# Kernel optimization log

Hardware: AMD Instinct MI355X
Metric: run time of the kernel (lower is better)

## Reference

```python
import jax, jax.numpy as jnp
import numpy as np

T, D, FF, E, R = 4096, 1024, 2048, 4, 16
LORA_SCALE = 32.0 / 16.0  # alpha / r


def setup_inputs() -> dict:
    key = jax.random.key(0)
    ks = jax.random.split(key, 12)
    return {
        "x": jax.random.normal(ks[0], (T, D), jnp.float32),
        "gate_w": jax.random.normal(ks[1], (E, D), jnp.float32) * 0.03,
        "gate_up_w": jax.random.normal(ks[2], (D, 2 * FF), jnp.float32)[None].repeat(E, 0) * 0.0
                     + jax.random.normal(ks[2], (E, D, 2 * FF), jnp.float32) * 0.03,
        "gate_up_b": jax.random.normal(ks[3], (E, 2 * FF), jnp.float32) * 0.01,
        "down_w": jax.random.normal(ks[4], (E, FF, D), jnp.float32) * 0.02,
        "down_b": jax.random.normal(ks[5], (E, D), jnp.float32) * 0.01,
        "A_gate": jax.random.normal(ks[6], (E, R, D), jnp.float32) * 0.02,
        "B_gate": jax.random.normal(ks[7], (E, FF, R), jnp.float32) * 0.02,
        "A_up": jax.random.normal(ks[8], (E, R, D), jnp.float32) * 0.02,
        "B_up": jax.random.normal(ks[9], (E, FF, R), jnp.float32) * 0.02,
        "A_down": jax.random.normal(ks[10], (E, R, FF), jnp.float32) * 0.02,
        "B_down": jax.random.normal(ks[11], (E, D, R), jnp.float32) * 0.02,
        "top_k": 2,
    }


def reference(x, gate_w, gate_up_w, gate_up_b, down_w, down_b,
              A_gate, B_gate, A_up, B_up, A_down, B_down, top_k):
    t, d = x.shape
    e = gate_w.shape[0]
    # --- router: logits, softmax (fp32), top-k, renormalize ---
    router_logits = x @ gate_w.T                                   # [T,E]
    rw = jax.nn.softmax(router_logits.astype(jnp.float32), axis=1)
    top_w, sel = jax.lax.top_k(rw, top_k)                          # [T,k]
    top_w = top_w / jnp.sum(top_w, axis=-1, keepdims=True)
    top_w = top_w.astype(x.dtype)
    # dense per-token per-expert combine weights (scatter of top-k weights)
    w = jnp.zeros((t, e), x.dtype).at[jnp.arange(t)[:, None], sel].add(top_w)  # [T,E]
    # --- per-expert SwiGLU MLP with LoRA (vectorized over experts) ---
    gu = jnp.einsum('td,edf->etf', x, gate_up_w) + gate_up_b[:, None, :]       # [E,T,2FF]
    ff = gu.shape[-1] // 2
    gate = gu[..., :ff] + jnp.einsum('td,erd,efr->etf', x, A_gate, B_gate) * LORA_SCALE
    up = gu[..., ff:] + jnp.einsum('td,erd,efr->etf', x, A_up, B_up) * LORA_SCALE
    act = jax.nn.silu(gate) * up                                               # [E,T,FF]
    down = jnp.einsum('etf,efd->etd', act, down_w) + down_b[:, None, :]
    down = down + jnp.einsum('etf,erf,edr->etd', act, A_down, B_down) * LORA_SCALE
    # --- weighted scatter-combine ---
    final = jnp.einsum('etd,te->td', down, w)                                  # [T,D]
    return final, router_logits
```

## Files before the change

kernel.cpp:

```cpp
#include <hip/hip_runtime.h>

#define T_TOK 4096
#define DIM   1024
#define FFD   2048
#define NEXP  4
#define NRP   8704
#define MTILES 68

typedef unsigned short u16;
typedef __attribute__((ext_vector_type(8))) short short8;
typedef __attribute__((ext_vector_type(4))) float f32x4;
typedef __attribute__((ext_vector_type(8))) unsigned short u16x8;
typedef __attribute__((ext_vector_type(4))) unsigned short u16x4;

typedef __attribute__((address_space(1))) unsigned int as1_u32;
typedef __attribute__((address_space(3))) unsigned int as3_u32;

__device__ __forceinline__ u16 f2bf(float f) {
  union { float f; unsigned u; } v; v.f = f;
  unsigned u = v.u;
  return (u16)((u + 0x7fffu + ((u >> 16) & 1u)) >> 16);
}
__device__ __forceinline__ float bf2f(u16 h) {
  union { unsigned u; float f; } v; v.u = ((unsigned)h) << 16;
  return v.f;
}
__device__ __forceinline__ void gload16(const void* g, void* l) {
  __builtin_amdgcn_global_load_lds((const as1_u32*)g, (as3_u32*)l, 16, 0, 0);
}

__global__ void router_k(const float* __restrict__ x, const float* __restrict__ gw,
                         float* __restrict__ logits_out, int* __restrict__ sel,
                         float* __restrict__ selw) {
  int t = blockIdx.x;
  int lane = threadIdx.x;
  float xv[16];
#pragma unroll
  for (int i = 0; i < 16; ++i) xv[i] = x[(size_t)t * DIM + lane + i * 64];
  float l[4];
#pragma unroll
  for (int e = 0; e < 4; ++e) {
    float s = 0.f;
#pragma unroll
    for (int i = 0; i < 16; ++i) s += xv[i] * gw[e * DIM + lane + i * 64];
#pragma unroll
    for (int off = 32; off > 0; off >>= 1) s += __shfl_xor(s, off, 64);
    l[e] = s;
  }
  if (lane == 0) {
#pragma unroll
    for (int e = 0; e < 4; ++e) logits_out[(size_t)t * 4 + e] = l[e];
    int e0 = 0; float b0 = l[0];
    for (int e = 1; e < 4; ++e) if (l[e] > b0) { b0 = l[e]; e0 = e; }
    int e1 = -1; float b1 = -3.4e38f;
    for (int e = 0; e < 4; ++e) if (e != e0 && l[e] > b1) { b1 = l[e]; e1 = e; }
    float p1 = expf(b1 - b0);
    float w0 = 1.f / (1.f + p1);
    sel[2 * t] = e0; sel[2 * t + 1] = e1;
    selw[2 * t] = w0; selw[2 * t + 1] = 1.f - w0;
  }
}

__global__ void scan_k(const int* __restrict__ sel, int* __restrict__ pos,
                       int* __restrict__ offs, int* __restrict__ rowtok,
                       int* __restrict__ pairrow) {
  __shared__ int base[4];
  __shared__ int wsum[16];
  __shared__ int off_s[5];
  int tid = threadIdx.x, lane = tid & 63, wid = tid >> 6;
  if (tid < 4) base[tid] = 0;
  __syncthreads();
  for (int chunk = 0; chunk < 4; ++chunk) {
    int t = chunk * 1024 + tid;
    int e0 = sel[2 * t], e1 = sel[2 * t + 1];
    for (int e = 0; e < 4; ++e) {
      bool f = (e0 == e) || (e1 == e);
      unsigned long long m = __ballot(f);
      int within = __popcll(m & ((1ull << lane) - 1ull));
      if (lane == 0) wsum[wid] = __popcll(m);
      __syncthreads();
      int wbase = 0, tot = 0;
      for (int i = 0; i < 16; ++i) { int v = wsum[i]; if (i < wid) wbase += v; tot += v; }
      if (f) {
        int p = base[e] + wbase + within;
        if (e0 == e) pos[2 * t] = p; else pos[2 * t + 1] = p;
      }
      __syncthreads();
      if (tid == 0) base[e] += tot;
      __syncthreads();
    }
  }
  if (tid == 0) {
    int o = 0;
    for (int e = 0; e < 4; ++e) { off_s[e] = o; o += ((base[e] + 127) >> 7) << 7; }
    off_s[4] = o;
    for (int i = 0; i < 5; ++i) offs[i] = off_s[i];
  }
  __syncthreads();
  for (int r = tid; r < NRP; r += 1024) rowtok[r] = -1;
  __syncthreads();
  for (int t = tid; t < T_TOK; t += 1024) {
#pragma unroll
    for (int s = 0; s < 2; ++s) {
      int e = sel[2 * t + s];
      int rr = off_s[e] + pos[2 * t + s];
      pairrow[2 * t + s] = rr;
      rowtok[rr] = t;
    }
  }
}

__global__ void gather_k(const float* __restrict__ x, const int* __restrict__ rowtok,
                         u16* __restrict__ xg) {
  int r = blockIdx.x, tid = threadIdx.x;
  int t = rowtok[r];
  float4 v = make_float4(0.f, 0.f, 0.f, 0.f);
  if (t >= 0) v = ((const float4*)(x + (size_t)t * DIM))[tid];
  u16x4 o;
  o[0] = f2bf(v.x); o[1] = f2bf(v.y); o[2] = f2bf(v.z); o[3] = f2bf(v.w);
  ((u16x4*)(xg + (size_t)r * DIM))[tid] = o;
}

__global__ void cvtA_k(const float* __restrict__ Ag, const float* __restrict__ Au,
                       const float* __restrict__ Ad, u16* __restrict__ abgu,
                       u16* __restrict__ adb) {
  int g = blockIdx.x * 256 + threadIdx.x;
  if (g < 32768) {
    int flat = g * 4;
    int e = flat >> 15;
    int rem = flat & 32767;
    int q = rem >> 10;
    int d = rem & 1023;
    const float* src = (q < 16) ? (Ag + ((size_t)e * 16 + q) * DIM + d)
                                : (Au + ((size_t)e * 16 + (q - 16)) * DIM + d);
    float4 v = *(const float4*)src;
    u16x4 o; o[0] = f2bf(v.x); o[1] = f2bf(v.y); o[2] = f2bf(v.z); o[3] = f2bf(v.w);
    *(u16x4*)(abgu + (size_t)flat) = o;
  } else {
    int flat = (g - 32768) * 4;
    float4 v = *(const float4*)(Ad + flat);
    u16x4 o; o[0] = f2bf(v.x); o[1] = f2bf(v.y); o[2] = f2bf(v.z); o[3] = f2bf(v.w);
    *(u16x4*)(adb + (size_t)flat) = o;
  }
}

__global__ void xa_k(const u16* __restrict__ xg, const u16* __restrict__ abgu,
                     const int* __restrict__ offs, float* __restrict__ xagu) {
  int r0 = blockIdx.x * 2, lane = threadIdx.x;
  int e = 0;
  if (r0 >= offs[1]) e = 1;
  if (r0 >= offs[2]) e = 2;
  if (r0 >= offs[3]) e = 3;
  float x0[16], x1[16];
#pragma unroll
  for (int i = 0; i < 4; ++i) {
    u16x4 v0 = ((const u16x4*)(xg + (size_t)r0 * DIM))[lane + i * 64];
    u16x4 v1 = ((const u16x4*)(xg + (size_t)(r0 + 1) * DIM))[lane + i * 64];
#pragma unroll
    for (int j = 0; j < 4; ++j) { x0[i * 4 + j] = bf2f(v0[j]); x1[i * 4 + j] = bf2f(v1[j]); }
  }
  const u16* A = abgu + (size_t)e * 32 * DIM;
  for (int q = 0; q < 32; ++q) {
    float s0 = 0.f, s1 = 0.f;
#pragma unroll
    for (int i = 0; i < 4; ++i) {
      u16x4 av = ((const u16x4*)(A + (size_t)q * DIM))[lane + i * 64];
#pragma unroll
      for (int j = 0; j < 4; ++j) {
        float a = bf2f(av[j]);
        s0 += x0[i * 4 + j] * a; s1 += x1[i * 4 + j] * a;
      }
    }
#pragma unroll
    for (int off = 32; off > 0; off >>= 1) { s0 += __shfl_xor(s0, off, 64); s1 += __shfl_xor(s1, off, 64); }
    if (lane == 0) { xagu[(size_t)r0 * 32 + q] = s0; xagu[(size_t)(r0 + 1) * 32 + q] = s1; }
  }
}

__global__ void aad_k(const u16* __restrict__ act, const u16* __restrict__ adb,
                      const int* __restrict__ offs, float* __restrict__ aad) {
  int r0 = blockIdx.x * 2, lane = threadIdx.x;
  int e = 0;
  if (r0 >= offs[1]) e = 1;
  if (r0 >= offs[2]) e = 2;
  if (r0 >= offs[3]) e = 3;
  float x0[32], x1[32];
#pragma unroll
  for (int i = 0; i < 8; ++i) {
    u16x4 v0 = ((const u16x4*)(act + (size_t)r0 * FFD))[lane + i * 64];
    u16x4 v1 = ((const u16x4*)(act + (size_t)(r0 + 1) * FFD))[lane + i * 64];
#pragma unroll
    for (int j = 0; j < 4; ++j) { x0[i * 4 + j] = bf2f(v0[j]); x1[i * 4 + j] = bf2f(v1[j]); }
  }
  const u16* A = adb + (size_t)e * 16 * FFD;
  for (int q = 0; q < 16; ++q) {
    float s0 = 0.f, s1 = 0.f;
#pragma unroll
    for (int i = 0; i < 8; ++i) {
      u16x4 av = ((const u16x4*)(A + (size_t)q * FFD))[lane + i * 64];
#pragma unroll
      for (int j = 0; j < 4; ++j) {
        float a = bf2f(av[j]);
        s0 += x0[i * 4 + j] * a; s1 += x1[i * 4 + j] * a;
      }
    }
#pragma unroll
    for (int off = 32; off > 0; off >>= 1) { s0 += __shfl_xor(s0, off, 64); s1 += __shfl_xor(s1, off, 64); }
    if (lane == 0) { aad[(size_t)r0 * 16 + q] = s0; aad[(size_t)(r0 + 1) * 16 + q] = s1; }
  }
}

__global__ void transpose_k(const float* __restrict__ in, u16* __restrict__ out,
                            int K, int N) {
  int e = blockIdx.z;
  int n0 = blockIdx.x * 32, k0 = blockIdx.y * 32;
  const float* I = in + (size_t)e * K * N;
  u16* O = out + (size_t)e * N * K;
  __shared__ u16 tile[32][33];
#pragma unroll
  for (int i = 0; i < 4; ++i) {
    int k = k0 + threadIdx.y + i * 8;
    tile[threadIdx.y + i * 8][threadIdx.x] = f2bf(I[(size_t)k * N + n0 + threadIdx.x]);
  }
  __syncthreads();
#pragma unroll
  for (int i = 0; i < 4; ++i) {
    int n = n0 + threadIdx.y + i * 8;
    O[(size_t)n * K + k0 + threadIdx.x] = tile[threadIdx.x][threadIdx.y + i * 8];
  }
}

__global__ __launch_bounds__(256) void gemm1_k(
    const u16* __restrict__ xg, const u16* __restrict__ wgu_t,
    const float* __restrict__ gub, const float* __restrict__ Bg,
    const float* __restrict__ Bu, const float* __restrict__ xagu,
    const int* __restrict__ offs, u16* __restrict__ act) {
  __shared__ __align__(16) u16 sAB[16384];
  int tid = threadIdx.x, w = tid >> 6, lane = tid & 63;
  int f0 = blockIdx.x * 64;
  int row0 = blockIdx.y * 128;
  int e = 0;
  if (row0 >= offs[1]) e = 1;
  if (row0 >= offs[2]) e = 2;
  if (row0 >= offs[3]) e = 3;

  int srow = w * 32 + (lane >> 2);
  int scol = ((lane & 3) ^ ((lane >> 3) & 3)) * 8;
  const u16* gA = xg + (size_t)(row0 + srow) * DIM + scol;
  int n1 = srow, n2 = srow + 16;
  int gr1 = (n1 < 64) ? (f0 + n1) : (2048 + f0 + n1 - 64);
  int gr2 = (n2 < 64) ? (f0 + n2) : (2048 + f0 + n2 - 64);
  const u16* gB1 = wgu_t + ((size_t)e << 22) + (size_t)gr1 * DIM + scol;
  const u16* gB2 = wgu_t + ((size_t)e << 22) + (size_t)gr2 * DIM + scol;
  int fo = (((lane >> 4) ^ ((lane >> 1) & 3))) * 8;
  int ar = (w * 32 + (lane & 15)) * 32 + fo;

  f32x4 acc[2][8];
#pragma unroll
  for (int i = 0; i < 2; ++i)
#pragma unroll
    for (int j = 0; j < 8; ++j) acc[i][j] = f32x4{0.f, 0.f, 0.f, 0.f};

  {
    u16* dA = sAB + w * 1024;
    u16* dB = sAB + 4096 + w * 1024;
    gload16(gA, dA); gload16(gA + 16 * DIM, dA + 512);
    gload16(gB1, dB); gload16(gB2, dB + 512);
  }
  __syncthreads();
  for (int t = 0; t < 31; ++t) {
    int b = t & 1;
    {
      int kk = (t + 1) * 32;
      u16* dA = sAB + (1 - b) * 8192 + w * 1024;
      u16* dB = sAB + (1 - b) * 8192 + 4096 + w * 1024;
      gload16(gA + kk, dA); gload16(gA + 16 * DIM + kk, dA + 512);
      gload16(gB1 + kk, dB); gload16(gB2 + kk, dB + 512);
    }
    {
      const u16* cA = sAB + b * 8192;
      const u16* cB = sAB + b * 8192 + 4096;
      short8 a[2], bb[8];
#pragma unroll
      for (int mi = 0; mi < 2; ++mi)
        a[mi] = *(const short8*)&cA[ar + mi * 512];
#pragma unroll
      for (int ni = 0; ni < 8; ++ni)
        bb[ni] = *(const short8*)&cB[(ni * 16 + (lane & 15)) * 32 + fo];
#pragma unroll
      for (int mi = 0; mi < 2; ++mi)
#pragma unroll
        for (int ni = 0; ni < 8; ++ni)
          acc[mi][ni] = __builtin_amdgcn_mfma_f32_16x16x32_bf16(a[mi], bb[ni], acc[mi][ni], 0, 0, 0);
    }
    __syncthreads();
  }
  {
    const u16* cA = sAB + 8192;
    const u16* cB = sAB + 8192 + 4096;
    short8 a[2], bb[8];
#pragma unroll
    for (int mi = 0; mi < 2; ++mi)
      a[mi] = *(const short8*)&cA[ar + mi * 512];
#pragma unroll
    for (int ni = 0; ni < 8; ++ni)
      bb[ni] = *(const short8*)&cB[(ni * 16 + (lane & 15)) * 32 + fo];
#pragma unroll
    for (int mi = 0; mi < 2; ++mi)
#pragma unroll
      for (int ni = 0; ni < 8; ++ni)
        acc[mi][ni] = __builtin_amdgcn_mfma_f32_16x16x32_bf16(a[mi], bb[ni], acc[mi][ni], 0, 0, 0);
  }

  u16* sA = sAB;
  u16* sB = sAB + 4096;
  __syncthreads();
  {
    int r = tid >> 1, kh = tid & 1;
    int sw = (r >> 1) & 3;
    int o0 = r * 32 + ((2 * kh + 0) ^ sw) * 8;
    int o1 = r * 32 + ((2 * kh + 1) ^ sw) * 8;
    u16 tmp[16];
    if (kh == 0) {
#pragma unroll
      for (int q = 0; q < 16; ++q) tmp[q] = f2bf(2.f * xagu[(size_t)(row0 + r) * 32 + q]);
    } else {
#pragma unroll
      for (int q = 0; q < 16; ++q) tmp[q] = 0;
      tmp[0] = 0x3f80;
    }
    *(u16x8*)&sA[o0] = *(u16x8*)&tmp[0];
    *(u16x8*)&sA[o1] = *(u16x8*)&tmp[8];
    int f = (r < 64) ? (f0 + r) : (f0 + r - 64);
    const float* Bsrc = (r < 64) ? Bg : Bu;
    float bias = gub[e * 4096 + ((r < 64) ? f : (2048 + f))];
    if (kh == 0) {
#pragma unroll
      for (int q = 0; q < 16; ++q) tmp[q] = f2bf(Bsrc[((size_t)e * FFD + f) * 16 + q]);
    } else {
#pragma unroll
      for (int q = 0; q < 16; ++q) tmp[q] = 0;
      tmp[0] = f2bf(bias);
    }
    *(u16x8*)&sB[o0] = *(u16x8*)&tmp[0];
    *(u16x8*)&sB[o1] = *(u16x8*)&tmp[8];
  }
  __syncthreads();
  {
    short8 a[2], b[4];
#pragma unroll
    for (int mi = 0; mi < 2; ++mi)
      a[mi] = *(const short8*)&sA[ar + mi * 512];
#pragma unroll
    for (int ni = 0; ni < 4; ++ni)
      b[ni] = *(const short8*)&sB[(ni * 16 + (lane & 15)) * 32 + fo];
#pragma unroll
    for (int mi = 0; mi < 2; ++mi)
#pragma unroll
      for (int ni = 0; ni < 4; ++ni)
        acc[mi][ni] = __builtin_amdgcn_mfma_f32_16x16x32_bf16(a[mi], b[ni], acc[mi][ni], 0, 0, 0);
  }
  __syncthreads();
  {
    int r = tid >> 1, kh = tid & 1;
    int sw = (r >> 1) & 3;
    int o0 = r * 32 + ((2 * kh + 0) ^ sw) * 8;
    int o1 = r * 32 + ((2 * kh + 1) ^ sw) * 8;
    u16 tmp[16];
    if (kh == 0) {
#pragma unroll
      for (int q = 0; q < 16; ++q) tmp[q] = f2bf(2.f * xagu[(size_t)(row0 + r) * 32 + 16 + q]);
    } else {
#pragma unroll
      for (int q = 0; q < 16; ++q) tmp[q] = 0;
      tmp[0] = 0x3f80;
    }
    *(u16x8*)&sA[o0] = *(u16x8*)&tmp[0];
    *(u16x8*)&sA[o1] = *(u16x8*)&tmp[8];
  }
  __syncthreads();
  {
    short8 a[2], b[4];
#pragma unroll
    for (int mi = 0; mi < 2; ++mi)
      a[mi] = *(const short8*)&sA[ar + mi * 512];
#pragma unroll
    for (int ni = 0; ni < 4; ++ni)
      b[ni] = *(const short8*)&sB[((ni + 4) * 16 + (lane & 15)) * 32 + fo];
#pragma unroll
    for (int mi = 0; mi < 2; ++mi)
#pragma unroll
      for (int ni = 0; ni < 4; ++ni)
        acc[mi][ni + 4] = __builtin_amdgcn_mfma_f32_16x16x32_bf16(a[mi], b[ni], acc[mi][ni + 4], 0, 0, 0);
  }
  __syncthreads();
#pragma unroll
  for (int mi = 0; mi < 2; ++mi)
#pragma unroll
    for (int ni = 0; ni < 4; ++ni)
#pragma unroll
      for (int j = 0; j < 4; ++j) {
        int lr = w * 32 + mi * 16 + (lane >> 4) * 4 + j;
        int lc = ni * 16 + (lane & 15);
        float g = acc[mi][ni][j];
        float u = acc[mi][ni + 4][j];
        float s = g / (1.f + __expf(-g));
        sAB[lr * 64 + lc] = f2bf(s * u);
      }
  __syncthreads();
#pragma unroll
  for (int it = 0; it < 4; ++it) {
    int idx = it * 256 + tid;
    int rr = idx >> 3, c8 = (idx & 7) * 8;
    *(u16x8*)(act + (size_t)(row0 + rr) * FFD + f0 + c8) = *(const u16x8*)&sAB[rr * 64 + c8];
  }
}

__global__ __launch_bounds__(256) void gemm2_k(
    const u16* __restrict__ act, const u16* __restrict__ wd_t,
    const float* __restrict__ db, const float* __restrict__ Bd,
    const float* __restrict__ aad, const int* __restrict__ offs,
    u16* __restrict__ down) {
  __shared__ __align__(16) u16 sAB[16384];
  int tid = threadIdx.x, w = tid >> 6, lane = tid & 63;
  int n0 = blockIdx.x * 128;
  int row0 = blockIdx.y * 128;
  int ks = blockIdx.z;
  size_t kbase = (size_t)ks * 1024;
  int e = 0;
  if (row0 >= offs[1]) e = 1;
  if (row0 >= offs[2]) e = 2;
  if (row0 >= offs[3]) e = 3;
  int wm = w >> 1, wn = w & 1;

  int srow = w * 32 + (lane >> 2);
  int scol = ((lane & 3) ^ ((lane >> 3) & 3)) * 8;
  const u16* gA = act + (size_t)(row0 + srow) * FFD + kbase + scol;
  const u16* gB = wd_t + (size_t)e * DIM * FFD + (size_t)(n0 + srow) * FFD + kbase + scol;
  int fo = (((lane >> 4) ^ ((lane >> 1) & 3))) * 8;
  int ar = (wm * 64 + (lane & 15)) * 32 + fo;
  int br = (wn * 64 + (lane & 15)) * 32 + fo;

  f32x4 acc[4][4];
#pragma unroll
  for (int i = 0; i < 4; ++i)
#pragma unroll
    for (int j = 0; j < 4; ++j) acc[i][j] = f32x4{0.f, 0.f, 0.f, 0.f};

  {
    u16* dA = sAB + w * 1024;
    u16* dB = sAB + 4096 + w * 1024;
    gload16(gA, dA); gload16(gA + 16 * FFD, dA + 512);
    gload16(gB, dB); gload16(gB + 16 * FFD, dB + 512);
  }
  __syncthreads();
  for (int t = 0; t < 31; ++t) {
    int b = t & 1;
    {
      int kk = (t + 1) * 32;
      u16* dA = sAB + (1 - b) * 8192 + w * 1024;
      u16* dB = sAB + (1 - b) * 8192 + 4096 + w * 1024;
      gload16(gA + kk, dA); gload16(gA + 16 * FFD + kk, dA + 512);
      gload16(gB + kk, dB); gload16(gB + 16 * FFD + kk, dB + 512);
    }
    {
      const u16* cA = sAB + b * 8192;
      const u16* cB = sAB + b * 8192 + 4096;
      short8 a[4], bb[4];
#pragma unroll
      for (int mi = 0; mi < 4; ++mi)
        a[mi] = *(const short8*)&cA[ar + mi * 512];
#pragma unroll
      for (int ni = 0; ni < 4; ++ni)
        bb[ni] = *(const short8*)&cB[br + ni * 512];
#pragma unroll
      for (int mi = 0; mi < 4; ++mi)
#pragma unroll
        for (int ni = 0; ni < 4; ++ni)
          acc[mi][ni] = __builtin_amdgcn_mfma_f32_16x16x32_bf16(a[mi], bb[ni], acc[mi][ni], 0, 0, 0);
    }
    __syncthreads();
  }
  {
    const u16* cA = sAB + 8192;
    const u16* cB = sAB + 8192 + 4096;
    short8 a[4], bb[4];
#pragma unroll
    for (int mi = 0; mi < 4; ++mi)
      a[mi] = *(const short8*)&cA[ar + mi * 512];
#pragma unroll
    for (int ni = 0; ni < 4; ++ni)
      bb[ni] = *(const short8*)&cB[br + ni * 512];
#pragma unroll
    for (int mi = 0; mi < 4; ++mi)
#pragma unroll
      for (int ni = 0; ni < 4; ++ni)
        acc[mi][ni] = __builtin_amdgcn_mfma_f32_16x16x32_bf16(a[mi], bb[ni], acc[mi][ni], 0, 0, 0);
  }

  u16* sA = sAB;
  u16* sB = sAB + 4096;
  if (ks == 0) {
    __syncthreads();
    {
      int r = tid >> 1, kh = tid & 1;
      int sw = (r >> 1) & 3;
      int o0 = r * 32 + ((2 * kh + 0) ^ sw) * 8;
      int o1 = r * 32 + ((2 * kh + 1) ^ sw) * 8;
      u16 tmp[16];
      if (kh == 0) {
#pragma unroll
        for (int q = 0; q < 16; ++q) tmp[q] = f2bf(2.f * aad[(size_t)(row0 + r) * 16 + q]);
      } else {
#pragma unroll
        for (int q = 0; q < 16; ++q) tmp[q] = 0;
        tmp[0] = 0x3f80;
      }
      *(u16x8*)&sA[o0] = *(u16x8*)&tmp[0];
      *(u16x8*)&sA[o1] = *(u16x8*)&tmp[8];
      if (kh == 0) {
#pragma unroll
        for (int q = 0; q < 16; ++q) tmp[q] = f2bf(Bd[((size_t)e * DIM + n0 + r) * 16 + q]);
      } else {
#pragma unroll
        for (int q = 0; q < 16; ++q) tmp[q] = 0;
        tmp[0] = f2bf(db[e * DIM + n0 + r]);
      }
      *(u16x8*)&sB[o0] = *(u16x8*)&tmp[0];
      *(u16x8*)&sB[o1] = *(u16x8*)&tmp[8];
    }
    __syncthreads();
    {
      short8 a[4], b[4];
#pragma unroll
      for (int mi = 0; mi < 4; ++mi)
        a[mi] = *(const short8*)&sA[ar + mi * 512];
#pragma unroll
      for (int ni = 0; ni < 4; ++ni)
        b[ni] = *(const short8*)&sB[br + ni * 512];
#pragma unroll
      for (int mi = 0; mi < 4; ++mi)
#pragma unroll
        for (int ni = 0; ni < 4; ++ni)
          acc[mi][ni] = __builtin_amdgcn_mfma_f32_16x16x32_bf16(a[mi], b[ni], acc[mi][ni], 0, 0, 0);
    }
  }
#pragma unroll
  for (int mi = 0; mi < 4; ++mi)
#pragma unroll
    for (int ni = 0; ni < 4; ++ni)
#pragma unroll
      for (int j = 0; j < 4; ++j) {
        int lr = wm * 64 + mi * 16 + (lane >> 4) * 4 + j;
        int lc = wn * 64 + ni * 16 + (lane & 15);
        down[((size_t)ks * NRP + row0 + lr) * DIM + n0 + lc] = f2bf(acc[mi][ni][j]);
      }
}

__global__ void combine_k(const u16* __restrict__ down, const int* __restrict__ pairrow,
                          const float* __restrict__ selw, float* __restrict__ out) {
  int t = blockIdx.x, tid = threadIdx.x;
  int r0 = pairrow[2 * t], r1 = pairrow[2 * t + 1];
  float w0 = selw[2 * t], w1 = selw[2 * t + 1];
  u16x4 a0 = *(const u16x4*)(down + ((size_t)r0) * DIM + tid * 4);
  u16x4 a1 = *(const u16x4*)(down + ((size_t)NRP + r0) * DIM + tid * 4);
  u16x4 b0 = *(const u16x4*)(down + ((size_t)r1) * DIM + tid * 4);
  u16x4 b1 = *(const u16x4*)(down + ((size_t)NRP + r1) * DIM + tid * 4);
  f32x4 o;
#pragma unroll
  for (int j = 0; j < 4; ++j)
    o[j] = w0 * (bf2f(a0[j]) + bf2f(a1[j])) + w1 * (bf2f(b0[j]) + bf2f(b1[j]));
  *(f32x4*)(out + (size_t)t * DIM + tid * 4) = o;
}

extern "C" void kernel_launch(void* const* d_in, const int* in_sizes, int n_in,
                              void* d_out, int out_size, void* d_ws, size_t ws_size,
                              hipStream_t stream) {
  const float* x         = (const float*)d_in[0];
  const float* gate_w    = (const float*)d_in[1];
  const float* gate_up_w = (const float*)d_in[2];
  const float* gate_up_b = (const float*)d_in[3];
  const float* down_w    = (const float*)d_in[4];
  const float* down_b    = (const float*)d_in[5];
  const float* A_gate    = (const float*)d_in[6];
  const float* B_gate    = (const float*)d_in[7];
  const float* A_up      = (const float*)d_in[8];
  const float* B_up      = (const float*)d_in[9];
  const float* A_down    = (const float*)d_in[10];
  const float* B_down    = (const float*)d_in[11];

  float* out_final  = (float*)d_out;
  float* out_logits = out_final + (size_t)T_TOK * DIM;

  char* ws = (char*)d_ws;
  size_t o = 0;
  auto take = [&](size_t bytes) -> void* {
    void* p = ws + o;
    o = (o + bytes + 255) & ~(size_t)255;
    return p;
  };
  int*   offs    = (int*)take(64);
  int*   sel     = (int*)take((size_t)T_TOK * 2 * 4);
  float* selw    = (float*)take((size_t)T_TOK * 2 * 4);
  int*   pos     = (int*)take((size_t)T_TOK * 2 * 4);
  int*   pairrow = (int*)take((size_t)T_TOK * 2 * 4);
  int*   rowtok  = (int*)take((size_t)NRP * 4);
  float* xagu    = (float*)take((size_t)NRP * 32 * 4);
  float* aadb    = (float*)take((size_t)NRP * 16 * 4);
  u16*   abgu    = (u16*)take((size_t)NEXP * 32 * DIM * 2);
  u16*   adb     = (u16*)take((size_t)NEXP * 16 * FFD * 2);
  u16*   xg      = (u16*)take((size_t)NRP * DIM * 2);
  u16*   actb    = (u16*)take((size_t)NRP * FFD * 2);
  u16*   downb   = (u16*)take((size_t)2 * NRP * DIM * 2);
  u16*   wgu_t   = (u16*)take((size_t)NEXP * 2 * FFD * DIM * 2);
  u16*   wd_t    = (u16*)take((size_t)NEXP * DIM * FFD * 2);
  (void)ws_size; (void)in_sizes; (void)n_in; (void)out_size;

  transpose_k<<<dim3(128, 32, NEXP), dim3(32, 8), 0, stream>>>(gate_up_w, wgu_t, DIM, 2 * FFD);
  transpose_k<<<dim3(32, 64, NEXP), dim3(32, 8), 0, stream>>>(down_w, wd_t, FFD, DIM);
  cvtA_k<<<256, 256, 0, stream>>>(A_gate, A_up, A_down, abgu, adb);

  router_k<<<T_TOK, 64, 0, stream>>>(x, gate_w, out_logits, sel, selw);
  scan_k<<<1, 1024, 0, stream>>>(sel, pos, offs, rowtok, pairrow);
  gather_k<<<NRP, 256, 0, stream>>>(x, rowtok, xg);
  xa_k<<<NRP / 2, 64, 0, stream>>>(xg, abgu, offs, xagu);
  gemm1_k<<<dim3(32, MTILES), 256, 0, stream>>>(xg, wgu_t, gate_up_b, B_gate, B_up,
                                                xagu, offs, actb);
  aad_k<<<NRP / 2, 64, 0, stream>>>(actb, adb, offs, aadb);
  gemm2_k<<<dim3(8, MTILES, 2), 256, 0, stream>>>(actb, wd_t, down_b, B_down, aadb, offs, downb);
  combine_k<<<T_TOK, 256, 0, stream>>>(downb, pairrow, selw, out_final);
}
```

Baseline: 289.7 us.

## Triple-buffer GEMM k-loop with vmcnt-based waits and batch scan ballots

Both grouped GEMM kernels move from double-buffered LDS staging to a three-stage ring. Loads are issued two k-steps ahead, and a partial s_waitcnt vmcnt plus s_barrier replaces the full __syncthreads, so global-to-LDS latency overlaps more MFMA work. The scan kernel also computes all four expert ballots before one shared reduction, cutting barriers per chunk from twelve to three. The cost is 48KB of LDS per block instead of 32KB, which may lower occupancy, and a fully unrolled loop with hand-written waitcnt barriers that depends on the compiler's memory-op counts.

New measurement: 272.4 us. 1.06x faster.

```diff
diff --git a/kernel.cpp b/kernel.cpp
--- a/kernel.cpp
+++ b/kernel.cpp
@@ -65,7 +65,7 @@
                        int* __restrict__ offs, int* __restrict__ rowtok,
                        int* __restrict__ pairrow) {
   __shared__ int base[4];
-  __shared__ int wsum[16];
+  __shared__ int wsum[16][4];
   __shared__ int off_s[5];
   int tid = threadIdx.x, lane = tid & 63, wid = tid >> 6;
   if (tid < 4) base[tid] = 0;
@@ -73,22 +73,33 @@
   for (int chunk = 0; chunk < 4; ++chunk) {
     int t = chunk * 1024 + tid;
     int e0 = sel[2 * t], e1 = sel[2 * t + 1];
+    unsigned long long ltm = (1ull << lane) - 1ull;
+    bool f[4]; int within[4];
+#pragma unroll
     for (int e = 0; e < 4; ++e) {
-      bool f = (e0 == e) || (e1 == e);
-      unsigned long long m = __ballot(f);
-      int within = __popcll(m & ((1ull << lane) - 1ull));
-      if (lane == 0) wsum[wid] = __popcll(m);
-      __syncthreads();
-      int wbase = 0, tot = 0;
-      for (int i = 0; i < 16; ++i) { int v = wsum[i]; if (i < wid) wbase += v; tot += v; }
-      if (f) {
-        int p = base[e] + wbase + within;
+      f[e] = (e0 == e) || (e1 == e);
+      unsigned long long m = __ballot(f[e]);
+      within[e] = __popcll(m & ltm);
+      if (lane == 0) wsum[wid][e] = __popcll(m);
+    }
+    __syncthreads();
+    int wbase[4] = {0, 0, 0, 0}, tot[4] = {0, 0, 0, 0};
+    for (int i = 0; i < 16; ++i)
+#pragma unroll
+      for (int e = 0; e < 4; ++e) {
+        int v = wsum[i][e];
+        if (i < wid) wbase[e] += v;
+        tot[e] += v;
+      }
+#pragma unroll
+    for (int e = 0; e < 4; ++e)
+      if (f[e]) {
+        int p = base[e] + wbase[e] + within[e];
         if (e0 == e) pos[2 * t] = p; else pos[2 * t + 1] = p;
       }
-      __syncthreads();
-      if (tid == 0) base[e] += tot;
-      __syncthreads();
-    }
+    __syncthreads();
+    if (tid < 4) base[tid] += tot[tid];
+    __syncthreads();
   }
   if (tid == 0) {
     int o = 0;
@@ -235,7 +246,7 @@
     const float* __restrict__ gub, const float* __restrict__ Bg,
     const float* __restrict__ Bu, const float* __restrict__ xagu,
     const int* __restrict__ offs, u16* __restrict__ act) {
-  __shared__ __align__(16) u16 sAB[16384];
+  __shared__ __align__(16) u16 sAB[24576];
   int tid = threadIdx.x, w = tid >> 6, lane = tid & 63;
   int f0 = blockIdx.x * 64;
   int row0 = blockIdx.y * 128;
@@ -247,6 +258,7 @@
   int srow = w * 32 + (lane >> 2);
   int scol = ((lane & 3) ^ ((lane >> 3) & 3)) * 8;
   const u16* gA = xg + (size_t)(row0 + srow) * DIM + scol;
+  const u16* gA2 = gA + 16 * DIM;
   int n1 = srow, n2 = srow + 16;
   int gr1 = (n1 < 64) ? (f0 + n1) : (2048 + f0 + n1 - 64);
   int gr2 = (n2 < 64) ? (f0 + n2) : (2048 + f0 + n2 - 64);
@@ -262,42 +274,25 @@
     for (int j = 0; j < 8; ++j) acc[i][j] = f32x4{0.f, 0.f, 0.f, 0.f};
 
   {
-    u16* dA = sAB + w * 1024;
-    u16* dB = sAB + 4096 + w * 1024;
-    gload16(gA, dA); gload16(gA + 16 * DIM, dA + 512);
-    gload16(gB1, dB); gload16(gB2, dB + 512);
-  }
-  __syncthreads();
-  for (int t = 0; t < 31; ++t) {
-    int b = t & 1;
-    {
-      int kk = (t + 1) * 32;
-      u16* dA = sAB + (1 - b) * 8192 + w * 1024;
-      u16* dB = sAB + (1 - b) * 8192 + 4096 + w * 1024;
-      gload16(gA + kk, dA); gload16(gA + 16 * DIM + kk, dA + 512);
-      gload16(gB1 + kk, dB); gload16(gB2 + kk, dB + 512);
-    }
-    {
-      const u16* cA = sAB + b * 8192;
-      const u16* cB = sAB + b * 8192 + 4096;
-      short8 a[2], bb[8];
-#pragma unroll
-      for (int mi = 0; mi < 2; ++mi)
-        a[mi] = *(const short8*)&cA[ar + mi * 512];
-#pragma unroll
-      for (int ni = 0; ni < 8; ++ni)
-        bb[ni] = *(const short8*)&cB[(ni * 16 + (lane & 15)) * 32 + fo];
-#pragma unroll
-      for (int mi = 0; mi < 2; ++mi)
-#pragma unroll
-        for (int ni = 0; ni < 8; ++ni)
-          acc[mi][ni] = __builtin_amdgcn_mfma_f32_16x16x32_bf16(a[mi], bb[ni], acc[mi][ni], 0, 0, 0);
-    }
-    __syncthreads();
-  }
-  {
-    const u16* cA = sAB + 8192;
-    const u16* cB = sAB + 8192 + 4096;
+    u16* d0 = sAB + w * 1024;
+    gload16(gA, d0); gload16(gA2, d0 + 512);
+    gload16(gB1, d0 + 4096); gload16(gB2, d0 + 4608);
+    u16* d1 = sAB + 8192 + w * 1024;
+    gload16(gA + 32, d1); gload16(gA2 + 32, d1 + 512);
+    gload16(gB1 + 32, d1 + 4096); gload16(gB2 + 32, d1 + 4608);
+  }
+#pragma unroll
+  for (int t = 0; t < 32; ++t) {
+    if (t == 31) asm volatile("s_waitcnt vmcnt(0)\n\ts_barrier" ::: "memory");
+    else         asm volatile("s_waitcnt vmcnt(4)\n\ts_barrier" ::: "memory");
+    if (t < 30) {
+      int kk = (t + 2) * 32;
+      u16* dA = sAB + ((t + 2) % 3) * 8192 + w * 1024;
+      gload16(gA + kk, dA); gload16(gA2 + kk, dA + 512);
+      gload16(gB1 + kk, dA + 4096); gload16(gB2 + kk, dA + 4608);
+    }
+    const u16* cA = sAB + (t % 3) * 8192;
+    const u16* cB = cA + 4096;
     short8 a[2], bb[8];
 #pragma unroll
     for (int mi = 0; mi < 2; ++mi)
@@ -421,7 +416,7 @@
     const float* __restrict__ db, const float* __restrict__ Bd,
     const float* __restrict__ aad, const int* __restrict__ offs,
     u16* __restrict__ down) {
-  __shared__ __align__(16) u16 sAB[16384];
+  __shared__ __align__(16) u16 sAB[24576];
   int tid = threadIdx.x, w = tid >> 6, lane = tid & 63;
   int n0 = blockIdx.x * 128;
   int row0 = blockIdx.y * 128;
@@ -436,7 +431,9 @@
   int srow = w * 32 + (lane >> 2);
   int scol = ((lane & 3) ^ ((lane >> 3) & 3)) * 8;
   const u16* gA = act + (size_t)(row0 + srow) * FFD + kbase + scol;
+  const u16* gA2 = gA + 16 * FFD;
   const u16* gB = wd_t + (size_t)e * DIM * FFD + (size_t)(n0 + srow) * FFD + kbase + scol;
+  const u16* gB2 = gB + 16 * FFD;
   int fo = (((lane >> 4) ^ ((lane >> 1) & 3))) * 8;
   int ar = (wm * 64 + (lane & 15)) * 32 + fo;
   int br = (wn * 64 + (lane & 15)) * 32 + fo;
@@ -448,42 +445,25 @@
     for (int j = 0; j < 4; ++j) acc[i][j] = f32x4{0.f, 0.f, 0.f, 0.f};
 
   {
-    u16* dA = sAB + w * 1024;
-    u16* dB = sAB + 4096 + w * 1024;
-    gload16(gA, dA); gload16(gA + 16 * FFD, dA + 512);
-    gload16(gB, dB); gload16(gB + 16 * FFD, dB + 512);
-  }
-  __syncthreads();
-  for (int t = 0; t < 31; ++t) {
-    int b = t & 1;
-    {
-      int kk = (t + 1) * 32;
-      u16* dA = sAB + (1 - b) * 8192 + w * 1024;
-      u16* dB = sAB + (1 - b) * 8192 + 4096 + w * 1024;
-      gload16(gA + kk, dA); gload16(gA + 16 * FFD + kk, dA + 512);
-      gload16(gB + kk, dB); gload16(gB + 16 * FFD + kk, dB + 512);
-    }
-    {
-      const u16* cA = sAB + b * 8192;
-      const u16* cB = sAB + b * 8192 + 4096;
-      short8 a[4], bb[4];
-#pragma unroll
-      for (int mi = 0; mi < 4; ++mi)
-        a[mi] = *(const short8*)&cA[ar + mi * 512];
-#pragma unroll
-      for (int ni = 0; ni < 4; ++ni)
-        bb[ni] = *(const short8*)&cB[br + ni * 512];
-#pragma unroll
-      for (int mi = 0; mi < 4; ++mi)
-#pragma unroll
-        for (int ni = 0; ni < 4; ++ni)
-          acc[mi][ni] = __builtin_amdgcn_mfma_f32_16x16x32_bf16(a[mi], bb[ni], acc[mi][ni], 0, 0, 0);
-    }
-    __syncthreads();
-  }
-  {
-    const u16* cA = sAB + 8192;
-    const u16* cB = sAB + 8192 + 4096;
+    u16* d0 = sAB + w * 1024;
+    gload16(gA, d0); gload16(gA2, d0 + 512);
+    gload16(gB, d0 + 4096); gload16(gB2, d0 + 4608);
+    u16* d1 = sAB + 8192 + w * 1024;
+    gload16(gA + 32, d1); gload16(gA2 + 32, d1 + 512);
+    gload16(gB + 32, d1 + 4096); gload16(gB2 + 32, d1 + 4608);
+  }
+#pragma unroll
+  for (int t = 0; t < 32; ++t) {
+    if (t == 31) asm volatile("s_waitcnt vmcnt(0)\n\ts_barrier" ::: "memory");
+    else         asm volatile("s_waitcnt vmcnt(4)\n\ts_barrier" ::: "memory");
+    if (t < 30) {
+      int kk = (t + 2) * 32;
+      u16* dA = sAB + ((t + 2) % 3) * 8192 + w * 1024;
+      gload16(gA + kk, dA); gload16(gA2 + kk, dA + 512);
+      gload16(gB + kk, dA + 4096); gload16(gB2 + kk, dA + 4608);
+    }
+    const u16* cA = sAB + (t % 3) * 8192;
+    const u16* cB = cA + 4096;
     short8 a[4], bb[4];
 #pragma unroll
     for (int mi = 0; mi < 4; ++mi)
```
